# Kernel optimization log

Hardware: AMD Instinct MI355X
Metric: run time of the kernel (lower is better)

The kernel has to match this reference:

```python
import jax, jax.numpy as jnp
import numpy as np
from math import pi as PI

L = 8192      # sequence length
D = 512       # feature dim
EMAS = 8      # number of decay rates


def setup_inputs() -> dict:
    key = jax.random.key(0)
    k1, _ = jax.random.split(key)
    x = jax.random.normal(k1, (L, D), dtype=jnp.float32)
    # module initializes log_decay = linspace(-pi, pi, emas)
    log_decay = jnp.linspace(-PI, PI, EMAS, dtype=jnp.float32)
    return {"x": x, "log_decay": log_decay}


def reference(x, log_decay):
    decay = jax.nn.sigmoid(log_decay)               # (emas,)
    # initial state: first element broadcast over emas -> (D, emas)
    state = jnp.broadcast_to(x[0][..., None], x.shape[1:] + (EMAS,))

    def ema_step(ema_0, x_1):
        ema_1 = decay * x_1 + (1.0 - decay) * ema_0
        return ema_1, ema_1

    # scan over l; carries (D, emas), xs is x[..., None] -> (L, D, 1) broadcast against decay
    _, ema_x = jax.lax.scan(ema_step, state, x[..., None])
    return ema_x  # (L, D, emas)
```

## Files before the change

kernel.cpp:

```cpp
#include <hip/hip_runtime.h>
#include <math.h>

#define L_  8192
#define D_  512
#define E_  8
#define DE_ 4096
#define C_  128
#define LC_ 64
#define ST_ 16

typedef float f4_t __attribute__((ext_vector_type(4)));

__device__ __forceinline__ float sigmoidf_(float v) {
    return 1.0f / (1.0f + expf(-v));
}

__global__ __launch_bounds__(256) void ema_pass1(const float* __restrict__ x,
                                                 const float* __restrict__ ld,
                                                 float* __restrict__ contrib) {
    const int c  = blockIdx.x >> 2;
    const int g  = ((blockIdx.x & 3) << 8) + threadIdx.x;
    const int d  = g >> 1;
    const int eb = (g & 1) << 2;

    float a[4], b[4];
#pragma unroll
    for (int e = 0; e < 4; ++e) { a[e] = sigmoidf_(ld[eb + e]); b[e] = 1.0f - a[e]; }

    float s[4] = {0.f, 0.f, 0.f, 0.f};
    const float* xp = x + (size_t)c * LC_ * D_ + d;

    float xs[2][ST_];
#pragma unroll
    for (int j = 0; j < ST_; ++j) xs[0][j] = xp[(size_t)j * D_];

#pragma unroll
    for (int st = 0; st < LC_ / ST_; ++st) {
        if (st + 1 < LC_ / ST_) {
#pragma unroll
            for (int j = 0; j < ST_; ++j)
                xs[(st + 1) & 1][j] = xp[(size_t)((st + 1) * ST_ + j) * D_];
        }
#pragma unroll
        for (int j = 0; j < ST_; ++j) {
            const float xv = xs[st & 1][j];
#pragma unroll
            for (int e = 0; e < 4; ++e) s[e] = fmaf(b[e], s[e], a[e] * xv);
        }
    }
    f4_t r = {s[0], s[1], s[2], s[3]};
    *(f4_t*)(contrib + (size_t)c * DE_ + 4 * g) = r;
}

__global__ __launch_bounds__(128) void ema_pass2(const float* __restrict__ x,
                                                 const float* __restrict__ ld,
                                                 const float* __restrict__ contrib,
                                                 float* __restrict__ states) {
    const int chain = blockIdx.x * 128 + threadIdx.x;
    const int d = chain >> 3;
    const int e = chain & 7;
    const float a = sigmoidf_(ld[e]);
    float B = 1.0f - a;
#pragma unroll
    for (int k = 0; k < 6; ++k) B *= B;

    float cb[2][ST_];
#pragma unroll
    for (int j = 0; j < ST_; ++j) cb[0][j] = contrib[(size_t)j * DE_ + chain];

    float s = x[d];
    states[chain] = s;

#pragma unroll
    for (int gr = 0; gr < C_ / ST_; ++gr) {
        if (gr + 1 < C_ / ST_) {
#pragma unroll
            for (int j = 0; j < ST_; ++j)
                cb[(gr + 1) & 1][j] = contrib[(size_t)((gr + 1) * ST_ + j) * DE_ + chain];
        }
#pragma unroll
        for (int j = 0; j < ST_; ++j) {
            s = fmaf(B, s, cb[gr & 1][j]);
            states[(size_t)(gr * ST_ + j + 1) * DE_ + chain] = s;
        }
    }
}

__global__ __launch_bounds__(256) void ema_pass3(const float* __restrict__ x,
                                                 const float* __restrict__ ld,
                                                 const float* __restrict__ states,
                                                 float* __restrict__ out) {
    const int c  = blockIdx.x >> 2;
    const int g  = ((blockIdx.x & 3) << 8) + threadIdx.x;
    const int d  = g >> 1;
    const int eb = (g & 1) << 2;

    float a[4], b[4];
#pragma unroll
    for (int e = 0; e < 4; ++e) { a[e] = sigmoidf_(ld[eb + e]); b[e] = 1.0f - a[e]; }

    f4_t y = *(const f4_t*)(states + (size_t)c * DE_ + 4 * g);
    const float* xp = x + (size_t)c * LC_ * D_ + d;
    float* op = out + (size_t)c * LC_ * DE_ + 4 * g;

    float xs[2][ST_];
#pragma unroll
    for (int j = 0; j < ST_; ++j) xs[0][j] = xp[(size_t)j * D_];

#pragma unroll
    for (int st = 0; st < LC_ / ST_; ++st) {
        if (st + 1 < LC_ / ST_) {
#pragma unroll
            for (int j = 0; j < ST_; ++j)
                xs[(st + 1) & 1][j] = xp[(size_t)((st + 1) * ST_ + j) * D_];
        }
#pragma unroll
        for (int j = 0; j < ST_; ++j) {
            const float xv = xs[st & 1][j];
            y.x = fmaf(b[0], y.x, a[0] * xv);
            y.y = fmaf(b[1], y.y, a[1] * xv);
            y.z = fmaf(b[2], y.z, a[2] * xv);
            y.w = fmaf(b[3], y.w, a[3] * xv);
            __builtin_nontemporal_store(y, (f4_t*)(op + (size_t)(st * ST_ + j) * DE_));
        }
    }
}

__global__ __launch_bounds__(256) void ema_naive(const float* __restrict__ x,
                                                 const float* __restrict__ ld,
                                                 float* __restrict__ out) {
    const int chain = blockIdx.x * 256 + threadIdx.x;
    const int d = chain >> 3;
    const int e = chain & 7;
    const float a = sigmoidf_(ld[e]);
    const float b = 1.0f - a;
    float y = x[d];
    for (int l = 0; l < L_; ++l) {
        y = fmaf(b, y, a * x[(size_t)l * D_ + d]);
        out[(size_t)l * DE_ + chain] = y;
    }
}

extern "C" void kernel_launch(void* const* d_in, const int* in_sizes, int n_in,
                              void* d_out, int out_size, void* d_ws, size_t ws_size,
                              hipStream_t stream) {
    const float* x  = (const float*)d_in[0];
    const float* ld = (const float*)d_in[1];
    float* out = (float*)d_out;

    const size_t need = (size_t)(2 * C_ + 1) * DE_ * sizeof(float);
    if (ws_size >= need) {
        float* contrib = (float*)d_ws;
        float* states  = contrib + (size_t)C_ * DE_;
        ema_pass1<<<C_ * 4, 256, 0, stream>>>(x, ld, contrib);
        ema_pass2<<<DE_ / 128, 128, 0, stream>>>(x, ld, contrib, states);
        ema_pass3<<<C_ * 4, 256, 0, stream>>>(x, ld, states, out);
    } else {
        ema_naive<<<DE_ / 256, 256, 0, stream>>>(x, ld, out);
    }
}
```

Baseline: 162.7 us.

## Stage x tiles through LDS with vector loads and rechunk into more, shorter chunks

Passes 1 and 3 now load their x tile into shared memory with coalesced float4 loads, replacing strided scalar per-thread global loads with register double-buffering. Chunks are halved to 32 rows, doubling the chunk count to 256, which gives more blocks in passes 1 and 3 but a longer sequential scan in pass 2. Pass 2 uses 64-thread blocks so that 64 blocks are spread across the device, and it prefetches 32 values per group. The cost is a longer serial dependency chain in pass 2 and twice the workspace traffic for contrib and states.

```diff
diff --git a/kernel.cpp b/kernel.cpp
--- a/kernel.cpp
+++ b/kernel.cpp
@@ -1,13 +1,15 @@
 #include <hip/hip_runtime.h>
 #include <math.h>
 
-#define L_  8192
-#define D_  512
-#define E_  8
-#define DE_ 4096
-#define C_  128
-#define LC_ 64
-#define ST_ 16
+#define L_   8192
+#define D_   512
+#define E_   8
+#define DE_  4096
+#define C_   256
+#define LC_  32
+#define TD_  128
+#define NF4_ (LC_ * TD_ / 4)
+#define P2B_ 64
 
 typedef float f4_t __attribute__((ext_vector_type(4)));
 
@@ -18,70 +20,69 @@
 __global__ __launch_bounds__(256) void ema_pass1(const float* __restrict__ x,
                                                  const float* __restrict__ ld,
                                                  float* __restrict__ contrib) {
-    const int c  = blockIdx.x >> 2;
-    const int g  = ((blockIdx.x & 3) << 8) + threadIdx.x;
-    const int d  = g >> 1;
+    __shared__ f4_t tile[NF4_];
+    const int c = blockIdx.x >> 2;
+    const int q = blockIdx.x & 3;
+    const int t = threadIdx.x;
+
+    const f4_t* xg = (const f4_t*)(x + (size_t)c * LC_ * D_ + q * TD_);
+#pragma unroll
+    for (int k = 0; k < 4; ++k) {
+        const int i = t + 256 * k;
+        tile[i] = xg[(size_t)(i >> 5) * (D_ / 4) + (i & 31)];
+    }
+
+    const int g  = (q << 8) + t;
+    const int dl = t >> 1;
     const int eb = (g & 1) << 2;
-
     float a[4], b[4];
 #pragma unroll
     for (int e = 0; e < 4; ++e) { a[e] = sigmoidf_(ld[eb + e]); b[e] = 1.0f - a[e]; }
 
+    __syncthreads();
+
+    const float* tl = (const float*)tile;
     float s[4] = {0.f, 0.f, 0.f, 0.f};
-    const float* xp = x + (size_t)c * LC_ * D_ + d;
-
-    float xs[2][ST_];
 #pragma unroll
-    for (int j = 0; j < ST_; ++j) xs[0][j] = xp[(size_t)j * D_];
-
+    for (int r = 0; r < LC_; ++r) {
+        const float xv = tl[r * TD_ + dl];
 #pragma unroll
-    for (int st = 0; st < LC_ / ST_; ++st) {
-        if (st + 1 < LC_ / ST_) {
-#pragma unroll
-            for (int j = 0; j < ST_; ++j)
-                xs[(st + 1) & 1][j] = xp[(size_t)((st + 1) * ST_ + j) * D_];
-        }
-#pragma unroll
-        for (int j = 0; j < ST_; ++j) {
-            const float xv = xs[st & 1][j];
-#pragma unroll
-            for (int e = 0; e < 4; ++e) s[e] = fmaf(b[e], s[e], a[e] * xv);
-        }
+        for (int e = 0; e < 4; ++e) s[e] = fmaf(b[e], s[e], a[e] * xv);
     }
-    f4_t r = {s[0], s[1], s[2], s[3]};
-    *(f4_t*)(contrib + (size_t)c * DE_ + 4 * g) = r;
+    f4_t rr = {s[0], s[1], s[2], s[3]};
+    *(f4_t*)(contrib + (size_t)c * DE_ + 4 * g) = rr;
 }
 
-__global__ __launch_bounds__(128) void ema_pass2(const float* __restrict__ x,
-                                                 const float* __restrict__ ld,
-                                                 const float* __restrict__ contrib,
-                                                 float* __restrict__ states) {
-    const int chain = blockIdx.x * 128 + threadIdx.x;
+__global__ __launch_bounds__(P2B_) void ema_pass2(const float* __restrict__ x,
+                                                  const float* __restrict__ ld,
+                                                  const float* __restrict__ contrib,
+                                                  float* __restrict__ states) {
+    const int chain = blockIdx.x * P2B_ + threadIdx.x;
     const int d = chain >> 3;
     const int e = chain & 7;
     const float a = sigmoidf_(ld[e]);
     float B = 1.0f - a;
 #pragma unroll
-    for (int k = 0; k < 6; ++k) B *= B;
+    for (int k = 0; k < 5; ++k) B *= B;
 
-    float cb[2][ST_];
+    float cb[2][32];
 #pragma unroll
-    for (int j = 0; j < ST_; ++j) cb[0][j] = contrib[(size_t)j * DE_ + chain];
+    for (int j = 0; j < 32; ++j) cb[0][j] = contrib[(size_t)j * DE_ + chain];
 
     float s = x[d];
     states[chain] = s;
 
 #pragma unroll
-    for (int gr = 0; gr < C_ / ST_; ++gr) {
-        if (gr + 1 < C_ / ST_) {
+    for (int gr = 0; gr < C_ / 32; ++gr) {
+        if (gr + 1 < C_ / 32) {
 #pragma unroll
-            for (int j = 0; j < ST_; ++j)
-                cb[(gr + 1) & 1][j] = contrib[(size_t)((gr + 1) * ST_ + j) * DE_ + chain];
+            for (int j = 0; j < 32; ++j)
+                cb[(gr + 1) & 1][j] = contrib[(size_t)((gr + 1) * 32 + j) * DE_ + chain];
         }
 #pragma unroll
-        for (int j = 0; j < ST_; ++j) {
+        for (int j = 0; j < 32; ++j) {
             s = fmaf(B, s, cb[gr & 1][j]);
-            states[(size_t)(gr * ST_ + j + 1) * DE_ + chain] = s;
+            states[(size_t)(gr * 32 + j + 1) * DE_ + chain] = s;
         }
     }
 }
@@ -90,39 +91,39 @@
                                                  const float* __restrict__ ld,
                                                  const float* __restrict__ states,
                                                  float* __restrict__ out) {
-    const int c  = blockIdx.x >> 2;
-    const int g  = ((blockIdx.x & 3) << 8) + threadIdx.x;
-    const int d  = g >> 1;
+    __shared__ f4_t tile[NF4_];
+    const int c = blockIdx.x >> 2;
+    const int q = blockIdx.x & 3;
+    const int t = threadIdx.x;
+
+    const f4_t* xg = (const f4_t*)(x + (size_t)c * LC_ * D_ + q * TD_);
+#pragma unroll
+    for (int k = 0; k < 4; ++k) {
+        const int i = t + 256 * k;
+        tile[i] = xg[(size_t)(i >> 5) * (D_ / 4) + (i & 31)];
+    }
+
+    const int g  = (q << 8) + t;
+    const int dl = t >> 1;
     const int eb = (g & 1) << 2;
-
     float a[4], b[4];
 #pragma unroll
     for (int e = 0; e < 4; ++e) { a[e] = sigmoidf_(ld[eb + e]); b[e] = 1.0f - a[e]; }
 
     f4_t y = *(const f4_t*)(states + (size_t)c * DE_ + 4 * g);
-    const float* xp = x + (size_t)c * LC_ * D_ + d;
     float* op = out + (size_t)c * LC_ * DE_ + 4 * g;
 
-    float xs[2][ST_];
+    __syncthreads();
+
+    const float* tl = (const float*)tile;
 #pragma unroll
-    for (int j = 0; j < ST_; ++j) xs[0][j] = xp[(size_t)j * D_];
-
-#pragma unroll
-    for (int st = 0; st < LC_ / ST_; ++st) {
-        if (st + 1 < LC_ / ST_) {
-#pragma unroll
-            for (int j = 0; j < ST_; ++j)
-                xs[(st + 1) & 1][j] = xp[(size_t)((st + 1) * ST_ + j) * D_];
-        }
-#pragma unroll
-        for (int j = 0; j < ST_; ++j) {
-            const float xv = xs[st & 1][j];
-            y.x = fmaf(b[0], y.x, a[0] * xv);
-            y.y = fmaf(b[1], y.y, a[1] * xv);
-            y.z = fmaf(b[2], y.z, a[2] * xv);
-            y.w = fmaf(b[3], y.w, a[3] * xv);
-            __builtin_nontemporal_store(y, (f4_t*)(op + (size_t)(st * ST_ + j) * DE_));
-        }
+    for (int r = 0; r < LC_; ++r) {
+        const float xv = tl[r * TD_ + dl];
+        y.x = fmaf(b[0], y.x, a[0] * xv);
+        y.y = fmaf(b[1], y.y, a[1] * xv);
+        y.z = fmaf(b[2], y.z, a[2] * xv);
+        y.w = fmaf(b[3], y.w, a[3] * xv);
+        __builtin_nontemporal_store(y, (f4_t*)(op + (size_t)r * DE_));
     }
 }
 
@@ -153,7 +154,7 @@
         float* contrib = (float*)d_ws;
         float* states  = contrib + (size_t)C_ * DE_;
         ema_pass1<<<C_ * 4, 256, 0, stream>>>(x, ld, contrib);
-        ema_pass2<<<DE_ / 128, 128, 0, stream>>>(x, ld, contrib, states);
+        ema_pass2<<<DE_ / P2B_, P2B_, 0, stream>>>(x, ld, contrib, states);
         ema_pass3<<<C_ * 4, 256, 0, stream>>>(x, ld, states, out);
     } else {
         ema_naive<<<DE_ / 256, 256, 0, stream>>>(x, ld, out);
```

After: 165.8 us. No clear change (+1.9%).
